# Performance work log

Hardware: AMD Instinct MI355X
Metric: run time of the kernel (lower is better)

Reference implementation:

```python
import jax, jax.numpy as jnp
import numpy as np

R, N, E, IN_DIM, HID, SEM_H = 3, 50000, 500000, 256, 128, 128


def setup_inputs() -> dict:
    key = jax.random.key(0)
    ks = jax.random.split(key, 20)
    s = 0.05
    return {
        # forward tensor args
        "dst_feat": jax.random.normal(ks[0], (N, IN_DIM), jnp.float32),
        "src_feats": jax.random.normal(ks[1], (R, N, IN_DIM), jnp.float32),
        "src_idx": jax.random.randint(ks[2], (R, E), 0, N, jnp.int32),
        "dst_idx": jax.random.randint(ks[3], (R, E), 0, N, jnp.int32),
        # weight_T: per-ntype projection in_dim -> hidden (dst ntype + R src ntypes, stacked)
        "WT_dst": jax.random.normal(ks[4], (IN_DIM, HID), jnp.float32) * s,
        "bT_dst": jnp.zeros((HID,), jnp.float32),
        "WT_src": jax.random.normal(ks[5], (R, IN_DIM, HID), jnp.float32) * s,
        "bT_src": jnp.zeros((R, HID), jnp.float32),
        # GATConv params per relation (1 head, shared fc for src/dst since in_feats is int)
        "W_gat": jax.random.normal(ks[6], (R, HID, HID), jnp.float32) * s,
        "attn_l": jax.random.normal(ks[7], (R, HID), jnp.float32) * s,
        "attn_r": jax.random.normal(ks[8], (R, HID), jnp.float32) * s,
        "b_gat": jnp.zeros((R, HID), jnp.float32),
        # SemanticAttention: Linear(HID,128)+tanh+Linear(128,1,no bias)
        "W1_sem": jax.random.normal(ks[9], (HID, SEM_H), jnp.float32) * s,
        "b1_sem": jnp.zeros((SEM_H,), jnp.float32),
        "w2_sem": jax.random.normal(ks[10], (SEM_H, 1), jnp.float32) * s,
    }


def reference(dst_feat, src_feats, src_idx, dst_idx,
              WT_dst, bT_dst, WT_src, bT_src,
              W_gat, attn_l, attn_r, b_gat,
              W1_sem, b1_sem, w2_sem):
    # weight_T projections (raw feat dim != hidden_dim branch)
    h_dst = dst_feat @ WT_dst + bT_dst                                  # [N, H]
    h_src = jnp.einsum('rni,rio->rno', src_feats, WT_src) + bT_src[:, None, :]  # [R, N, H]
    n_nodes = h_dst.shape[0]

    def gat(h_s_in, si, di, W, al, ar, b):
        # DGL GATConv, 1 head, eval mode (no dropout), shared fc for src/dst
        hs = h_s_in @ W                                                 # [N, H]
        hd = h_dst @ W                                                  # [N, H]
        el = (hs * al).sum(-1)                                          # [N]
        er = (hd * ar).sum(-1)                                          # [N]
        e = el[si] + er[di]                                             # [E]
        e = jnp.where(e > 0, e, 0.2 * e)                                # leaky_relu(0.2)
        # edge softmax segmented by destination node
        m = jax.ops.segment_max(e, di, num_segments=n_nodes)
        ex = jnp.exp(e - m[di])
        ssum = jax.ops.segment_sum(ex, di, num_segments=n_nodes)
        alpha = ex / ssum[di]                                           # [E]
        out = jax.ops.segment_sum(alpha[:, None] * hs[si], di, num_segments=n_nodes)  # [N, H]
        return jax.nn.elu(out + b)                                      # activation=F.elu, + bias

    z_r = jax.vmap(gat)(h_src, src_idx, dst_idx, W_gat, attn_l, attn_r, b_gat)  # [R, N, H]

    # SemanticAttention over relations
    z_m = jnp.transpose(z_r, (1, 0, 2))                                 # [N, R, H]
    w = jnp.tanh(z_m @ W1_sem + b1_sem) @ w2_sem                        # [N, R, 1]
    a = jax.nn.softmax(w.mean(axis=0), axis=0)                          # [R, 1]
    return (z_m * a).sum(axis=1)                                        # [N, H]
```

## Files before the change

### kernel.cpp

```cpp
#include <hip/hip_runtime.h>
#include <hip/hip_bf16.h>

#define R_REL 3
#define NODE_CHUNK 512
#define BCAP 6144

typedef __attribute__((ext_vector_type(8))) short bf16x8;
typedef __attribute__((ext_vector_type(4))) float f32x4;

static inline size_t align_up(size_t x, size_t a) { return (x + a - 1) & ~(a - 1); }

__device__ __forceinline__ float eluf(float x) {
    return x > 0.f ? x : (__expf(x) - 1.f);
}
__device__ __forceinline__ unsigned short f2bf(float f) {
    __hip_bfloat16 h = __float2bfloat16(f);
    return *reinterpret_cast<unsigned short*>(&h);
}
__device__ __forceinline__ unsigned pk2bf(float lo, float hi) {
    __hip_bfloat162 h = __float22bfloat162_rn(make_float2(lo, hi));
    return *reinterpret_cast<unsigned*>(&h);
}
__device__ __forceinline__ float bf2f(unsigned short h) {
    return __uint_as_float((unsigned)h << 16);
}


__global__ void vu_kernel(const float* __restrict__ W_gat, const float* __restrict__ attn_r,
                          const float* __restrict__ WT_dst, const float* __restrict__ bT_dst,
                          float* __restrict__ u, float* __restrict__ cc) {
    int r = blockIdx.x;
    int t = threadIdx.x;
    __shared__ float ar[128];
    __shared__ float vs[128];
    if (t < 128) ar[t] = attn_r[r * 128 + t];
    __syncthreads();
    if (t < 128) {
        const float* W = W_gat + (size_t)r * 128 * 128 + (size_t)t * 128;
        float s = 0.f;
        for (int j = 0; j < 128; ++j) s += W[j] * ar[j];
        vs[t] = s;
    }
    __syncthreads();
    const float* W = WT_dst + (size_t)t * 128;
    float s = 0.f;
    for (int i = 0; i < 128; ++i) s += W[i] * vs[i];
    u[r * 256 + t] = s;
    if (t == 0) {
        float c = 0.f;
        for (int i = 0; i < 128; ++i) c += bT_dst[i] * vs[i];
        cc[r] = c;
    }
}

__global__ void wc_kernel(const float* __restrict__ WT_src, const float* __restrict__ bT_src,
                          const float* __restrict__ W_gat, float* __restrict__ Wc,
                          float* __restrict__ bc) {
    int r = blockIdx.y;
    int k = blockIdx.x;
    int j = threadIdx.x;
    __shared__ float as[128];
    const float* arow = (k < 256) ? (WT_src + ((size_t)r * 256 + k) * 128)
                                  : (bT_src + (size_t)r * 128);
    as[j] = arow[j];
    __syncthreads();
    const float* W = W_gat + (size_t)r * 128 * 128;
    float s = 0.f;
    for (int i = 0; i < 128; ++i) s += as[i] * W[(size_t)i * 128 + j];
    if (k < 256) Wc[((size_t)r * 256 + k) * 128 + j] = s;
    else         bc[(size_t)r * 128 + j] = s;
}

__global__ void pack_kernel(const float* __restrict__ S, unsigned short* __restrict__ P,
                            int relstride, int KS) {
    int r = blockIdx.y;
    int ks = blockIdx.x >> 3, cb = blockIdx.x & 7;
    int l = threadIdx.x;
    const float* Sr = S + (size_t)r * relstride;
    int col = cb * 16 + (l & 15);
    int kb = ks * 32 + (l >> 4) * 8;
    unsigned short v[8];
#pragma unroll
    for (int j = 0; j < 8; ++j) v[j] = f2bf(Sr[(size_t)(kb + j) * 128 + col]);
    unsigned short* dst = P + ((((size_t)r * KS + ks) * 8 + cb) * 64 + l) * 8;
    *(uint4*)dst = *(uint4*)v;
}


__global__ __launch_bounds__(256) void gemm_hs(
    const float* __restrict__ src, const unsigned short* __restrict__ Bpack,
    const float* __restrict__ bc, const float* __restrict__ attn_l,
    unsigned short* __restrict__ hsb, float* __restrict__ el, int N) {
    const int r = blockIdx.y;
    const int t = threadIdx.x;
    const int w = t >> 6, l = t & 63;
    const int rowbase = blockIdx.x * 64 + w * 16;
    const int arow_i = rowbase + (l & 15);
    const int kg = l >> 4;
    const float* A = src + (size_t)r * N * 256;
    const float* arow = A + (size_t)(arow_i < N ? arow_i : N - 1) * 256;
    const bf16x8* bp = (const bf16x8*)(Bpack + (size_t)r * 256 * 128);
    f32x4 acc[8] = {};
#pragma unroll
    for (int ks = 0; ks < 8; ++ks) {
        float4 a0 = *(const float4*)(arow + ks * 32 + kg * 8);
        float4 a1 = *(const float4*)(arow + ks * 32 + kg * 8 + 4);
        uint4 uv;
        uv.x = pk2bf(a0.x, a0.y);
        uv.y = pk2bf(a0.z, a0.w);
        uv.z = pk2bf(a1.x, a1.y);
        uv.w = pk2bf(a1.z, a1.w);
        bf16x8 av = *(bf16x8*)&uv;
#pragma unroll
        for (int cf = 0; cf < 8; ++cf) {
            bf16x8 bv = bp[(ks * 8 + cf) * 64 + l];
            acc[cf] = __builtin_amdgcn_mfma_f32_16x16x32_bf16(av, bv, acc[cf], 0, 0, 0);
        }
    }
    float bcv[8], alv[8];
#pragma unroll
    for (int cf = 0; cf < 8; ++cf) {
        int col = cf * 16 + (l & 15);
        bcv[cf] = bc[r * 128 + col];
        alv[cf] = attn_l[r * 128 + col];
    }
#pragma unroll
    for (int i = 0; i < 4; ++i) {
        int row = rowbase + (l >> 4) * 4 + i;
        float pe = 0.f;
        unsigned short hv[8];
#pragma unroll
        for (int cf = 0; cf < 8; ++cf) {
            float v = acc[cf][i] + bcv[cf];
            pe += v * alv[cf];
            hv[cf] = f2bf(v);
        }
        if (row < N) {
            unsigned short* hp = hsb + ((size_t)r * N + row) * 128 + (l & 15);
#pragma unroll
            for (int cf = 0; cf < 8; ++cf) hp[cf * 16] = hv[cf];
        }
        pe += __shfl_xor(pe, 1, 64);
        pe += __shfl_xor(pe, 2, 64);
        pe += __shfl_xor(pe, 4, 64);
        pe += __shfl_xor(pe, 8, 64);
        if ((l & 15) == 0 && row < N) el[(size_t)r * N + row] = pe;
    }
}


__global__ void er_kernel(const float* __restrict__ dst_feat, const float* __restrict__ u,
                          const float* __restrict__ cc, float* __restrict__ er, int N) {
    __shared__ float us[3][256];
    for (int i = threadIdx.x; i < 3 * 256; i += 256) us[i / 256][i & 255] = u[i];
    __syncthreads();
    int wave = threadIdx.x >> 6, lane = threadIdx.x & 63;
    int n = blockIdx.x * 4 + wave;
    if (n >= N) return;
    float4 f = *(const float4*)(dst_feat + (size_t)n * 256 + lane * 4);
#pragma unroll
    for (int r = 0; r < R_REL; ++r) {
        float4 uv = *(float4*)&us[r][lane * 4];
        float s = f.x * uv.x + f.y * uv.y + f.z * uv.z + f.w * uv.w;
#pragma unroll
        for (int off = 32; off >= 1; off >>= 1) s += __shfl_xor(s, off, 64);
        if (lane == 0) er[(size_t)r * N + n] = s + cc[r];
    }
}


__global__ __launch_bounds__(256) void bucket_kernel(
    const int* __restrict__ si, const int* __restrict__ di,
    int* __restrict__ gcnt, unsigned* __restrict__ bbuf, int NB, int E) {
    const int r = blockIdx.y;
    const int t = threadIdx.x;
    const int e0 = blockIdx.x * 1024;
    __shared__ int cnt[128];
    __shared__ int base[128];
    if (t < 128) cnt[t] = 0;
    __syncthreads();
    int bk[4], rank[4]; unsigned pack[4]; bool val[4];
#pragma unroll
    for (int j = 0; j < 4; ++j) {
        int e = e0 + j * 256 + t;
        val[j] = e < E;
        bk[j] = 0; rank[j] = 0; pack[j] = 0;
        if (val[j]) {
            size_t g = (size_t)r * E + e;
            int s = si[g], d = di[g];
            bk[j] = d >> 9;
            pack[j] = (unsigned)s | ((unsigned)d << 16);
            rank[j] = atomicAdd(&cnt[bk[j]], 1);
        }
    }
    __syncthreads();
    if (t < NB && cnt[t] > 0) base[t] = atomicAdd(&gcnt[r * NB + t], cnt[t]);
    __syncthreads();
#pragma unroll
    for (int j = 0; j < 4; ++j) {
        if (val[j])
            bbuf[((size_t)r * NB + bk[j]) * BCAP + base[bk[j]] + rank[j]] = pack[j];
    }
}

__global__ __launch_bounds__(256) void hist_kernel(
    const unsigned* __restrict__ bbuf, const int* __restrict__ gcnt,
    int* __restrict__ deg, int NB, int N) {
    const int r = blockIdx.y;
    const int b = blockIdx.x;
    const int t = threadIdx.x;
    __shared__ int hist[NODE_CHUNK];
    for (int i = t; i < NODE_CHUNK; i += 256) hist[i] = 0;
    __syncthreads();
    const int cnt = gcnt[r * NB + b];
    const unsigned* bb = bbuf + ((size_t)r * NB + b) * BCAP;
    for (int i = t; i < cnt; i += 256) {
        int dloc = (bb[i] >> 16) & (NODE_CHUNK - 1);
        atomicAdd(&hist[dloc], 1);
    }
    __syncthreads();
    for (int i = t; i < NODE_CHUNK; i += 256) {
        int idx = b * NODE_CHUNK + i;
        if (idx < N) deg[(size_t)r * N + idx] = hist[i];
    }
}

__global__ __launch_bounds__(1024) void scan1_kernel(const int* __restrict__ deg,
                                                     int* __restrict__ offs,
                                                     int* __restrict__ btot, int N, int nchunk) {
    const int r = blockIdx.y;
    const int idx = blockIdx.x * 1024 + threadIdx.x;
    const int lane = threadIdx.x & 63, wave = threadIdx.x >> 6;
    __shared__ int wsum[16];
    int v = (idx < N) ? deg[(size_t)r * N + idx] : 0;
    int x = v;
#pragma unroll
    for (int off = 1; off < 64; off <<= 1) {
        int y = __shfl_up(x, off, 64);
        if (lane >= off) x += y;
    }
    if (lane == 63) wsum[wave] = x;
    __syncthreads();
    if (wave == 0 && lane < 16) {
        int y = wsum[lane];
#pragma unroll
        for (int off = 1; off < 16; off <<= 1) {
            int z = __shfl_up(y, off, 64);
            if (lane >= off) y += z;
        }
        wsum[lane] = y;
    }
    __syncthreads();
    int woff = (wave > 0) ? wsum[wave - 1] : 0;
    if (idx < N) offs[(size_t)r * N + idx] = woff + x - v;
    if (threadIdx.x == 1023) btot[r * nchunk + blockIdx.x] = woff + x;
}

__global__ __launch_bounds__(256) void scan2_kernel(const int* __restrict__ btot,
                                                    int* __restrict__ offs, int N, int nchunk) {
    const int r = blockIdx.y;
    const int chunk = blockIdx.x;
    const int t = threadIdx.x;
    const int lane = t & 63, wave = t >> 6;
    __shared__ int red[4];
    int pre = 0;
    for (int i = t; i < chunk; i += 256) pre += btot[r * nchunk + i];
#pragma unroll
    for (int off = 32; off >= 1; off >>= 1) pre += __shfl_xor(pre, off, 64);
    if (lane == 0) red[wave] = pre;
    __syncthreads();
    int ptot = red[0] + red[1] + red[2] + red[3];
    for (int j = t; j < 1024; j += 256) {
        int idx = chunk * 1024 + j;
        if (idx < N) offs[(size_t)r * N + idx] += ptot;
    }
}

__global__ __launch_bounds__(256) void fill2_kernel(
    const unsigned* __restrict__ bbuf, const int* __restrict__ gcnt,
    const int* __restrict__ offs, unsigned short* __restrict__ csr, int NB, int N, int E) {
    const int r = blockIdx.y;
    const int b = blockIdx.x;
    const int t = threadIdx.x;
    __shared__ int curl[NODE_CHUNK];
    for (int i = t; i < NODE_CHUNK; i += 256) {
        int idx = b * NODE_CHUNK + i;
        curl[i] = (idx < N) ? offs[(size_t)r * N + idx] : 0;
    }
    __syncthreads();
    const int cnt = gcnt[r * NB + b];
    const unsigned* bb = bbuf + ((size_t)r * NB + b) * BCAP;
    unsigned short* csrr = csr + (size_t)r * E;
    for (int i = t; i < cnt; i += 256) {
        unsigned pk = bb[i];
        int dloc = (pk >> 16) & (NODE_CHUNK - 1);
        int pos = atomicAdd(&curl[dloc], 1);
        csrr[pos] = (unsigned short)(pk & 0xffffu);
    }
}


__global__ __launch_bounds__(256) void gather_kernel(
    const unsigned short* __restrict__ csr, const int* __restrict__ offs,
    const int* __restrict__ deg, const float* __restrict__ el, const float* __restrict__ er,
    const unsigned short* __restrict__ hsb, const float* __restrict__ b_gat,
    unsigned short* __restrict__ z, int N, int E) {
    const int r = blockIdx.y;
    const int wid = threadIdx.x >> 6;
    const int l = threadIdx.x & 63;
    const int grp = l >> 4, gl = l & 15;
    const int d = blockIdx.x * 4 + wid;
    if (d >= N) return;
    const int beg = offs[(size_t)r * N + d];
    const int dg = deg[(size_t)r * N + d];
    float ac[8] = {0.f, 0.f, 0.f, 0.f, 0.f, 0.f, 0.f, 0.f};
    if (dg > 0) {
        const float erd = er[(size_t)r * N + d];
        const float* elr = el + (size_t)r * N;
        const unsigned short* csrr = csr + (size_t)r * E;
        const unsigned short* hsr = hsb + (size_t)r * N * 128;

        float ssum = 0.f;
        for (int c = beg; c < beg + dg; c += 64) {
            int nn = min(64, beg + dg - c);
            int pos = grp + gl * 4;
            int src = 0; float p = 0.f;
            if (pos < nn) {
                src = csrr[c + pos];
                float e = elr[src] + erd;
                e = e > 0.f ? e : 0.2f * e;
                p = __expf(e);
                ssum += p;
            }
            int ng = (nn - grp + 3) >> 2;
            for (int j = 0; j < ng; ++j) {
                float pj = __shfl(p, (l & 48) + j, 64);
                int sj = __shfl(src, (l & 48) + j, 64);
                uint4 hw = *(const uint4*)(hsr + (size_t)sj * 128 + gl * 8);
                ac[0] += pj * bf2f((unsigned short)(hw.x & 0xffffu));
                ac[1] += pj * bf2f((unsigned short)(hw.x >> 16));
                ac[2] += pj * bf2f((unsigned short)(hw.y & 0xffffu));
                ac[3] += pj * bf2f((unsigned short)(hw.y >> 16));
                ac[4] += pj * bf2f((unsigned short)(hw.z & 0xffffu));
                ac[5] += pj * bf2f((unsigned short)(hw.z >> 16));
                ac[6] += pj * bf2f((unsigned short)(hw.w & 0xffffu));
                ac[7] += pj * bf2f((unsigned short)(hw.w >> 16));
            }
        }
#pragma unroll
        for (int off = 1; off <= 32; off <<= 1) ssum += __shfl_xor(ssum, off, 64);
#pragma unroll
        for (int k = 0; k < 8; ++k) {
            ac[k] += __shfl_xor(ac[k], 16, 64);
            ac[k] += __shfl_xor(ac[k], 32, 64);
        }
        float inv = 1.f / ssum;
#pragma unroll
        for (int k = 0; k < 8; ++k) ac[k] *= inv;
    }
    if (grp == 0) {
        const float* bg = b_gat + r * 128 + gl * 8;
        uint4 ow;
        ow.x = pk2bf(eluf(ac[0] + bg[0]), eluf(ac[1] + bg[1]));
        ow.y = pk2bf(eluf(ac[2] + bg[2]), eluf(ac[3] + bg[3]));
        ow.z = pk2bf(eluf(ac[4] + bg[4]), eluf(ac[5] + bg[5]));
        ow.w = pk2bf(eluf(ac[6] + bg[6]), eluf(ac[7] + bg[7]));
        *(uint4*)(z + ((size_t)r * N + d) * 128 + gl * 8) = ow;
    }
}


__global__ __launch_bounds__(256) void gemm_sem(
    const unsigned short* __restrict__ z, const unsigned short* __restrict__ W1p,
    const float* __restrict__ b1, const float* __restrict__ w2,
    float* __restrict__ wpart, int N) {
    const int r = blockIdx.y;
    const int n0 = blockIdx.x * 64;
    const int t = threadIdx.x;
    const int w = t >> 6, l = t & 63;
    __shared__ unsigned short Alds[64 * 128];
    __shared__ float sred[4];
    const unsigned short* A = z + (size_t)r * N * 128;
#pragma unroll
    for (int i = 0; i < 4; ++i) {
        int cid = t + 256 * i;
        int row = cid >> 4, kc = cid & 15;
        uint4 v = make_uint4(0, 0, 0, 0);
        if (n0 + row < N) v = *(const uint4*)(A + (size_t)(n0 + row) * 128 + kc * 8);
        int off = ((row * 256) + kc * 16) ^ ((row & 7) << 4);
        *(uint4*)((char*)Alds + off) = v;
    }
    __syncthreads();

    const bf16x8* bp = (const bf16x8*)W1p;
    f32x4 acc[8] = {};
    const int arow = w * 16 + (l & 15);
#pragma unroll
    for (int ks = 0; ks < 4; ++ks) {
        int aoff = ((arow * 256) + ks * 64 + (l >> 4) * 16) ^ ((arow & 7) << 4);
        bf16x8 av = *(const bf16x8*)((char*)Alds + aoff);
#pragma unroll
        for (int cf = 0; cf < 8; ++cf) {
            bf16x8 bv = bp[(ks * 8 + cf) * 64 + l];
            acc[cf] = __builtin_amdgcn_mfma_f32_16x16x32_bf16(av, bv, acc[cf], 0, 0, 0);
        }
    }
    float b1v[8], w2v[8];
#pragma unroll
    for (int cf = 0; cf < 8; ++cf) {
        int col = cf * 16 + (l & 15);
        b1v[cf] = b1[col];
        w2v[cf] = w2[col];
    }
    float wloc = 0.f;
#pragma unroll
    for (int i = 0; i < 4; ++i) {
        int row = n0 + w * 16 + (l >> 4) * 4 + i;
        float s = 0.f;
#pragma unroll
        for (int cf = 0; cf < 8; ++cf) s += tanhf(acc[cf][i] + b1v[cf]) * w2v[cf];
        s += __shfl_xor(s, 1, 64);
        s += __shfl_xor(s, 2, 64);
        s += __shfl_xor(s, 4, 64);
        s += __shfl_xor(s, 8, 64);
        if ((l & 15) == 0 && row < N) wloc += s;
    }
    wloc += __shfl_xor(wloc, 16, 64);
    wloc += __shfl_xor(wloc, 32, 64);
    if (l == 0) sred[w] = wloc;
    __syncthreads();
    if (t == 0)
        wpart[(size_t)r * gridDim.x + blockIdx.x] = sred[0] + sred[1] + sred[2] + sred[3];
}


__global__ void reduce_sem(const float* __restrict__ wpart, float* __restrict__ aw,
                           int nblk, int N) {
    const int t = threadIdx.x, l = t & 63, w = t >> 6;
    __shared__ float sred[R_REL][4];
    float s[R_REL] = {0.f, 0.f, 0.f};
    for (int i = t; i < nblk; i += 256) {
#pragma unroll
        for (int r = 0; r < R_REL; ++r) s[r] += wpart[(size_t)r * nblk + i];
    }
#pragma unroll
    for (int r = 0; r < R_REL; ++r) {
#pragma unroll
        for (int off = 32; off >= 1; off >>= 1) s[r] += __shfl_xor(s[r], off, 64);
        if (l == 0) sred[r][w] = s[r];
    }
    __syncthreads();
    if (t == 0) {
        float w0 = (sred[0][0] + sred[0][1] + sred[0][2] + sred[0][3]) / (float)N;
        float w1 = (sred[1][0] + sred[1][1] + sred[1][2] + sred[1][3]) / (float)N;
        float w2 = (sred[2][0] + sred[2][1] + sred[2][2] + sred[2][3]) / (float)N;
        float m = fmaxf(w0, fmaxf(w1, w2));
        float e0 = __expf(w0 - m), e1 = __expf(w1 - m), e2 = __expf(w2 - m);
        float si = e0 + e1 + e2;
        aw[0] = e0 / si; aw[1] = e1 / si; aw[2] = e2 / si;
    }
}

__global__ void combine(const unsigned short* __restrict__ z, const float* __restrict__ aw,
                        float* __restrict__ out, int N) {
    int idx = blockIdx.x * 256 + threadIdx.x;
    if (idx >= N * 32) return;
    int n = idx >> 5, c4 = idx & 31;
    float a0 = aw[0], a1 = aw[1], a2 = aw[2];
    uint2 z0 = *(const uint2*)(z + ((size_t)0 * N + n) * 128 + c4 * 4);
    uint2 z1 = *(const uint2*)(z + ((size_t)1 * N + n) * 128 + c4 * 4);
    uint2 z2 = *(const uint2*)(z + ((size_t)2 * N + n) * 128 + c4 * 4);
    float4 o;
    o.x = a0 * bf2f((unsigned short)(z0.x & 0xffffu)) + a1 * bf2f((unsigned short)(z1.x & 0xffffu)) + a2 * bf2f((unsigned short)(z2.x & 0xffffu));
    o.y = a0 * bf2f((unsigned short)(z0.x >> 16))     + a1 * bf2f((unsigned short)(z1.x >> 16))     + a2 * bf2f((unsigned short)(z2.x >> 16));
    o.z = a0 * bf2f((unsigned short)(z0.y & 0xffffu)) + a1 * bf2f((unsigned short)(z1.y & 0xffffu)) + a2 * bf2f((unsigned short)(z2.y & 0xffffu));
    o.w = a0 * bf2f((unsigned short)(z0.y >> 16))     + a1 * bf2f((unsigned short)(z1.y >> 16))     + a2 * bf2f((unsigned short)(z2.y >> 16));
    *(float4*)(out + (size_t)idx * 4) = o;
}


extern "C" void kernel_launch(void* const* d_in, const int* in_sizes, int n_in,
                              void* d_out, int out_size, void* d_ws, size_t ws_size,
                              hipStream_t stream) {
    const float* dst_feat = (const float*)d_in[0];
    const float* src_feats = (const float*)d_in[1];
    const int*   src_idx  = (const int*)d_in[2];
    const int*   dst_idx  = (const int*)d_in[3];
    const float* WT_dst   = (const float*)d_in[4];
    const float* bT_dst   = (const float*)d_in[5];
    const float* WT_src   = (const float*)d_in[6];
    const float* bT_src   = (const float*)d_in[7];
    const float* W_gat    = (const float*)d_in[8];
    const float* attn_l   = (const float*)d_in[9];
    const float* attn_r   = (const float*)d_in[10];
    const float* b_gat    = (const float*)d_in[11];
    const float* W1_sem   = (const float*)d_in[12];
    const float* b1_sem   = (const float*)d_in[13];
    const float* w2_sem   = (const float*)d_in[14];

    const int N = in_sizes[0] / 256;
    const int E = in_sizes[2] / R_REL;
    float* out = (float*)d_out;

    const int nblk = (N + 63) / 64;
    const int nchunk = (N + 1023) / 1024;
    const int NB = (N + NODE_CHUNK - 1) / NODE_CHUNK;

    char* ws = (char*)d_ws;
    size_t off = 0;
    auto alloc = [&](size_t bytes) { char* p = ws + off; off = align_up(off + bytes, 256); return p; };
    unsigned short* hsb   = (unsigned short*)alloc((size_t)R_REL * N * 128 * 2);
    unsigned short* zbuf  = (unsigned short*)alloc((size_t)R_REL * N * 128 * 2);
    float*    Wc    = (float*)alloc((size_t)R_REL * 256 * 128 * 4);
    unsigned short* Wcp   = (unsigned short*)alloc((size_t)R_REL * 256 * 128 * 2);
    unsigned short* W1p   = (unsigned short*)alloc((size_t)128 * 128 * 2);
    float*    bc    = (float*)alloc(R_REL * 128 * 4);
    float*    u     = (float*)alloc(R_REL * 256 * 4);
    float*    cc    = (float*)alloc(R_REL * 4);
    float*    el    = (float*)alloc((size_t)R_REL * N * 4);
    float*    er    = (float*)alloc((size_t)R_REL * N * 4);
    int*      deg   = (int*)alloc((size_t)R_REL * N * 4);
    int*      offs  = (int*)alloc((size_t)R_REL * N * 4);
    int*      btot  = (int*)alloc((size_t)R_REL * nchunk * 4);
    int*      gcnt  = (int*)alloc((size_t)R_REL * NB * 4);
    unsigned* bbuf  = (unsigned*)alloc((size_t)R_REL * NB * BCAP * 4);
    unsigned short* csr = (unsigned short*)alloc((size_t)R_REL * E * 2);
    float*    wpart = (float*)alloc((size_t)R_REL * nblk * 4);
    float*    aw    = (float*)alloc(R_REL * 4);

    hipMemsetAsync(gcnt, 0, (size_t)R_REL * NB * 4, stream);

    vu_kernel<<<R_REL, 256, 0, stream>>>(W_gat, attn_r, WT_dst, bT_dst, u, cc);
    wc_kernel<<<dim3(257, R_REL), 128, 0, stream>>>(WT_src, bT_src, W_gat, Wc, bc);
    pack_kernel<<<dim3(64, R_REL), 64, 0, stream>>>(Wc, Wcp, 256 * 128, 8);
    pack_kernel<<<dim3(32, 1), 64, 0, stream>>>(W1_sem, W1p, 0, 4);

    bucket_kernel<<<dim3((E + 1023) / 1024, R_REL), 256, 0, stream>>>(src_idx, dst_idx, gcnt, bbuf, NB, E);
    hist_kernel<<<dim3(NB, R_REL), 256, 0, stream>>>(bbuf, gcnt, deg, NB, N);
    scan1_kernel<<<dim3(nchunk, R_REL), 1024, 0, stream>>>(deg, offs, btot, N, nchunk);
    scan2_kernel<<<dim3(nchunk, R_REL), 256, 0, stream>>>(btot, offs, N, nchunk);
    fill2_kernel<<<dim3(NB, R_REL), 256, 0, stream>>>(bbuf, gcnt, offs, csr, NB, N, E);

    dim3 g1(nblk, R_REL);
    gemm_hs<<<g1, 256, 0, stream>>>(src_feats, Wcp, bc, attn_l, hsb, el, N);
    er_kernel<<<(N + 3) / 4, 256, 0, stream>>>(dst_feat, u, cc, er, N);

    gather_kernel<<<dim3((N + 3) / 4, R_REL), 256, 0, stream>>>(csr, offs, deg, el, er, hsb, b_gat, zbuf, N, E);

    gemm_sem<<<g1, 256, 0, stream>>>(zbuf, W1p, b1_sem, w2_sem, wpart, N);
    reduce_sem<<<1, 256, 0, stream>>>(wpart, aw, nblk, N);
    combine<<<(N * 32 + 255) / 256, 256, 0, stream>>>(zbuf, aw, out, N);
}
```

Before: 284.1 us.

## Map one 16-lane group per destination node in gather and prefetch GEMM A rows

The gather kernel now gives each destination node to a 16-thread group instead of a full 64-lane wavefront, so each block handles 16 nodes. Each group walks its edges serially, and every lane recomputes the softmax weight itself, removing the shuffles and cross-group reductions. With an average degree of about 10, the old layout left most lanes idle, so this aims to use lanes better. Separately, gemm_hs loads and converts the whole A row into registers before the MFMA loop so the loads are issued together. The cost is more registers in gemm_hs, redundant el and exp work across the 16 lanes, and serialized per-edge memory latency in gather.

```diff
diff --git a/kernel.cpp b/kernel.cpp
--- a/kernel.cpp
+++ b/kernel.cpp
@@ -99,18 +99,27 @@
     const int kg = l >> 4;
     const float* A = src + (size_t)r * N * 256;
     const float* arow = A + (size_t)(arow_i < N ? arow_i : N - 1) * 256;
+
+    float4 araw[16];
+#pragma unroll
+    for (int ks = 0; ks < 8; ++ks) {
+        araw[2 * ks]     = *(const float4*)(arow + ks * 32 + kg * 8);
+        araw[2 * ks + 1] = *(const float4*)(arow + ks * 32 + kg * 8 + 4);
+    }
+    uint4 abf[8];
+#pragma unroll
+    for (int ks = 0; ks < 8; ++ks) {
+        abf[ks].x = pk2bf(araw[2 * ks].x, araw[2 * ks].y);
+        abf[ks].y = pk2bf(araw[2 * ks].z, araw[2 * ks].w);
+        abf[ks].z = pk2bf(araw[2 * ks + 1].x, araw[2 * ks + 1].y);
+        abf[ks].w = pk2bf(araw[2 * ks + 1].z, araw[2 * ks + 1].w);
+    }
+
     const bf16x8* bp = (const bf16x8*)(Bpack + (size_t)r * 256 * 128);
     f32x4 acc[8] = {};
 #pragma unroll
     for (int ks = 0; ks < 8; ++ks) {
-        float4 a0 = *(const float4*)(arow + ks * 32 + kg * 8);
-        float4 a1 = *(const float4*)(arow + ks * 32 + kg * 8 + 4);
-        uint4 uv;
-        uv.x = pk2bf(a0.x, a0.y);
-        uv.y = pk2bf(a0.z, a0.w);
-        uv.z = pk2bf(a1.x, a1.y);
-        uv.w = pk2bf(a1.z, a1.w);
-        bf16x8 av = *(bf16x8*)&uv;
+        bf16x8 av = *(bf16x8*)&abf[ks];
 #pragma unroll
         for (int cf = 0; cf < 8; ++cf) {
             bf16x8 bv = bp[(ks * 8 + cf) * 64 + l];
@@ -306,67 +315,43 @@
     const unsigned short* __restrict__ hsb, const float* __restrict__ b_gat,
     unsigned short* __restrict__ z, int N, int E) {
     const int r = blockIdx.y;
-    const int wid = threadIdx.x >> 6;
-    const int l = threadIdx.x & 63;
-    const int grp = l >> 4, gl = l & 15;
-    const int d = blockIdx.x * 4 + wid;
+    const int t = threadIdx.x;
+    const int gid = t >> 4;
+    const int gl = t & 15;
+    const int d = blockIdx.x * 16 + gid;
     if (d >= N) return;
     const int beg = offs[(size_t)r * N + d];
     const int dg = deg[(size_t)r * N + d];
     float ac[8] = {0.f, 0.f, 0.f, 0.f, 0.f, 0.f, 0.f, 0.f};
-    if (dg > 0) {
-        const float erd = er[(size_t)r * N + d];
-        const float* elr = el + (size_t)r * N;
-        const unsigned short* csrr = csr + (size_t)r * E;
-        const unsigned short* hsr = hsb + (size_t)r * N * 128;
-
-        float ssum = 0.f;
-        for (int c = beg; c < beg + dg; c += 64) {
-            int nn = min(64, beg + dg - c);
-            int pos = grp + gl * 4;
-            int src = 0; float p = 0.f;
-            if (pos < nn) {
-                src = csrr[c + pos];
-                float e = elr[src] + erd;
-                e = e > 0.f ? e : 0.2f * e;
-                p = __expf(e);
-                ssum += p;
-            }
-            int ng = (nn - grp + 3) >> 2;
-            for (int j = 0; j < ng; ++j) {
-                float pj = __shfl(p, (l & 48) + j, 64);
-                int sj = __shfl(src, (l & 48) + j, 64);
-                uint4 hw = *(const uint4*)(hsr + (size_t)sj * 128 + gl * 8);
-                ac[0] += pj * bf2f((unsigned short)(hw.x & 0xffffu));
-                ac[1] += pj * bf2f((unsigned short)(hw.x >> 16));
-                ac[2] += pj * bf2f((unsigned short)(hw.y & 0xffffu));
-                ac[3] += pj * bf2f((unsigned short)(hw.y >> 16));
-                ac[4] += pj * bf2f((unsigned short)(hw.z & 0xffffu));
-                ac[5] += pj * bf2f((unsigned short)(hw.z >> 16));
-                ac[6] += pj * bf2f((unsigned short)(hw.w & 0xffffu));
-                ac[7] += pj * bf2f((unsigned short)(hw.w >> 16));
-            }
-        }
-#pragma unroll
-        for (int off = 1; off <= 32; off <<= 1) ssum += __shfl_xor(ssum, off, 64);
-#pragma unroll
-        for (int k = 0; k < 8; ++k) {
-            ac[k] += __shfl_xor(ac[k], 16, 64);
-            ac[k] += __shfl_xor(ac[k], 32, 64);
-        }
-        float inv = 1.f / ssum;
-#pragma unroll
-        for (int k = 0; k < 8; ++k) ac[k] *= inv;
-    }
-    if (grp == 0) {
-        const float* bg = b_gat + r * 128 + gl * 8;
-        uint4 ow;
-        ow.x = pk2bf(eluf(ac[0] + bg[0]), eluf(ac[1] + bg[1]));
-        ow.y = pk2bf(eluf(ac[2] + bg[2]), eluf(ac[3] + bg[3]));
-        ow.z = pk2bf(eluf(ac[4] + bg[4]), eluf(ac[5] + bg[5]));
-        ow.w = pk2bf(eluf(ac[6] + bg[6]), eluf(ac[7] + bg[7]));
-        *(uint4*)(z + ((size_t)r * N + d) * 128 + gl * 8) = ow;
-    }
+    float ssum = 0.f;
+    const float erd = er[(size_t)r * N + d];
+    const float* elr = el + (size_t)r * N;
+    const unsigned short* csrr = csr + (size_t)r * E;
+    const unsigned short* hsr = hsb + (size_t)r * N * 128;
+    for (int i = beg; i < beg + dg; ++i) {
+        int src = csrr[i];
+        float e = elr[src] + erd;
+        e = e > 0.f ? e : 0.2f * e;
+        float p = __expf(e);
+        ssum += p;
+        uint4 hw = *(const uint4*)(hsr + (size_t)src * 128 + gl * 8);
+        ac[0] += p * bf2f((unsigned short)(hw.x & 0xffffu));
+        ac[1] += p * bf2f((unsigned short)(hw.x >> 16));
+        ac[2] += p * bf2f((unsigned short)(hw.y & 0xffffu));
+        ac[3] += p * bf2f((unsigned short)(hw.y >> 16));
+        ac[4] += p * bf2f((unsigned short)(hw.z & 0xffffu));
+        ac[5] += p * bf2f((unsigned short)(hw.z >> 16));
+        ac[6] += p * bf2f((unsigned short)(hw.w & 0xffffu));
+        ac[7] += p * bf2f((unsigned short)(hw.w >> 16));
+    }
+    float inv = (dg > 0) ? 1.f / ssum : 0.f;
+    const float* bg = b_gat + r * 128 + gl * 8;
+    uint4 ow;
+    ow.x = pk2bf(eluf(ac[0] * inv + bg[0]), eluf(ac[1] * inv + bg[1]));
+    ow.y = pk2bf(eluf(ac[2] * inv + bg[2]), eluf(ac[3] * inv + bg[3]));
+    ow.z = pk2bf(eluf(ac[4] * inv + bg[4]), eluf(ac[5] * inv + bg[5]));
+    ow.w = pk2bf(eluf(ac[6] * inv + bg[6]), eluf(ac[7] * inv + bg[7]));
+    *(uint4*)(z + ((size_t)r * N + d) * 128 + gl * 8) = ow;
 }
 
 
@@ -545,7 +530,7 @@
     gemm_hs<<<g1, 256, 0, stream>>>(src_feats, Wcp, bc, attn_l, hsb, el, N);
     er_kernel<<<(N + 3) / 4, 256, 0, stream>>>(dst_feat, u, cc, er, N);
 
-    gather_kernel<<<dim3((N + 3) / 4, R_REL), 256, 0, stream>>>(csr, offs, deg, el, er, hsb, b_gat, zbuf, N, E);
+    gather_kernel<<<dim3((N + 15) / 16, R_REL), 256, 0, stream>>>(csr, offs, deg, el, er, hsb, b_gat, zbuf, N, E);
 
     gemm_sem<<<g1, 256, 0, stream>>>(zbuf, W1p, b1_sem, w2_sem, wpart, N);
     reduce_sem<<<1, 256, 0, stream>>>(wpart, aw, nblk, N);
```

Result: faster. 266.2 us (-6.3%).
